# Kernel tuning notes

Hardware: AMD Instinct MI355X
Metric: run time of the kernel (lower is better)

Reference implementation:

```python
import jax, jax.numpy as jnp
import numpy as np

B, S, H, I, E = 2, 1024, 1024, 4096, 8

def setup_inputs() -> dict:
    key = jax.random.key(0)
    ks = jax.random.split(key, 8)
    s_h = 1.0 / np.sqrt(H)
    s_i = 1.0 / np.sqrt(I)
    return {
        "x": jax.random.normal(ks[0], (B, S, H), dtype=jnp.float32),
        "router_w": jax.random.uniform(ks[1], (H, E), jnp.float32, -s_h, s_h),
        "router_b": jax.random.uniform(ks[2], (E,), jnp.float32, -s_h, s_h),
        "w1": jax.random.uniform(ks[3], (E, H, I), jnp.float32, -s_h, s_h),
        "b1": jax.random.uniform(ks[4], (E, I), jnp.float32, -s_h, s_h),
        "w2": jax.random.uniform(ks[5], (E, I, H), jnp.float32, -s_i, s_i),
        "b2": jax.random.uniform(ks[6], (E, H), jnp.float32, -s_i, s_i),
        "game_emb": jax.random.normal(ks[7], (E, H), dtype=jnp.float32) * 0.02,
    }

def reference(x, router_w, router_b, w1, b1, w2, b2, game_emb):
    # Router: top-1 expert per token (softmax is monotone, argmax of logits)
    logits = jnp.einsum('bsh,he->bse', x, router_w) + router_b  # [B,S,E]
    expert_idx = jnp.argmax(logits, axis=-1)                    # [B,S] int
    out = jnp.zeros_like(x)
    n_experts = w1.shape[0]
    for e in range(n_experts):  # fixed small expert loop
        mask = (expert_idx == e)[..., None]                     # [B,S,1]
        sel = x + 0.1 * game_emb[e]                             # embedding add
        h = jax.nn.gelu(jnp.einsum('bsh,hi->bsi', sel, w1[e]) + b1[e], approximate=False)
        y = jnp.einsum('bsi,ih->bsh', h, w2[e]) + b2[e]
        out = jnp.where(mask, y, out)                           # scatter combine
    return out
```

## Files before the change

### kernel.cpp

```cpp
#include <hip/hip_runtime.h>
#include <hip/hip_bf16.h>
#include <math.h>

#define HDIM 1024
#define IDIM 4096
#define NE 8
#define NTOK 2048
#define PADROWS 256

typedef __attribute__((ext_vector_type(8))) short bf16x8;
typedef __attribute__((ext_vector_type(4))) float f32x4;

__device__ __forceinline__ unsigned int f2bf(float f) {
    unsigned int u = __float_as_uint(f);
    u = (u + 0x7FFFu + ((u >> 16) & 1u)) >> 16;
    return u;
}

__device__ __forceinline__ unsigned int pkbf2(float lo, float hi) {
    union { __hip_bfloat162 h; unsigned int u; } cv;
    cv.h = __float22bfloat162_rn(make_float2(lo, hi));
    return cv.u;
}

__device__ __forceinline__ float comp4(const float4& v, int c) {
    return c == 0 ? v.x : c == 1 ? v.y : c == 2 ? v.z : v.w;
}

__device__ __forceinline__ int swz8(int i) { return (i ^ (i >> 3)) & 7; }

__device__ __forceinline__ float gelu_erf(float v) {
    float x = v * 0.70710678118654752f;
    float ax = fabsf(x);
    float t = 1.0f / (1.0f + 0.3275911f * ax);
    float p = t * (0.254829592f + t * (-0.284496736f + t * (1.421413741f +
              t * (-1.453152027f + t * 1.061405429f))));
    float er = 1.0f - p * __expf(-x * x);
    er = copysignf(er, v);
    return 0.5f * v * (1.0f + er);
}

template<typename T, typename U>
__device__ __forceinline__ void gld16(const T* g, U* l) {
    __builtin_amdgcn_global_load_lds((const __attribute__((address_space(1))) void*)g,
                                     (__attribute__((address_space(3))) void*)l, 16, 0, 0);
}

__global__ __launch_bounds__(256) void router_k(const float* __restrict__ x,
                                                const float* __restrict__ rw,
                                                const float* __restrict__ rb,
                                                int* __restrict__ eidx,
                                                int* __restrict__ counts) {
    const int wave = threadIdx.x >> 6, lane = threadIdx.x & 63;
    const int t = blockIdx.x * 4 + wave;
    if (t >= NTOK) return;
    double acc[NE];
#pragma unroll
    for (int e = 0; e < NE; e++) acc[e] = 0.0;
    for (int h = lane; h < HDIM; h += 64) {
        double xv = (double)x[(size_t)t * HDIM + h];
        const float4* rwp = (const float4*)&rw[h * NE];
        float4 r0 = rwp[0], r1 = rwp[1];
        acc[0] += xv * (double)r0.x;  acc[1] += xv * (double)r0.y;
        acc[2] += xv * (double)r0.z;  acc[3] += xv * (double)r0.w;
        acc[4] += xv * (double)r1.x;  acc[5] += xv * (double)r1.y;
        acc[6] += xv * (double)r1.z;  acc[7] += xv * (double)r1.w;
    }
#pragma unroll
    for (int m = 32; m >= 1; m >>= 1) {
#pragma unroll
        for (int e = 0; e < NE; e++) acc[e] += __shfl_xor(acc[e], m);
    }
    if (lane == 0) {
        double best = acc[0] + (double)rb[0];
        int be = 0;
#pragma unroll
        for (int e = 1; e < NE; e++) {
            double v = acc[e] + (double)rb[e];
            if (v > best) { best = v; be = e; }
        }
        eidx[t] = be;
        atomicAdd(&counts[be], 1);
    }
}

__global__ void scan_k(const int* __restrict__ counts, int* __restrict__ offsets) {
    if (threadIdx.x == 0 && blockIdx.x == 0) {
        int s = 0;
        for (int e = 0; e < NE; e++) { offsets[e] = s; s += counts[e]; }
        offsets[NE] = s;
    }
}

__global__ __launch_bounds__(256) void gather_k(const float* __restrict__ x,
                                                const float* __restrict__ gemb,
                                                const int* __restrict__ eidx,
                                                const int* __restrict__ offsets,
                                                int* __restrict__ cursors,
                                                int* __restrict__ rowmap,
                                                unsigned short* __restrict__ Xg) {
    __shared__ int srow, se;
    const int t = blockIdx.x;
    if (threadIdx.x == 0) {
        int e = eidx[t];
        int pos = atomicAdd(&cursors[e], 1);
        int row = offsets[e] + pos;
        rowmap[row] = t;
        srow = row; se = e;
    }
    __syncthreads();
    const int row = srow, e = se;
    const int c = threadIdx.x * 4;
    float4 xv = *(const float4*)&x[(size_t)t * HDIM + c];
    float4 gv = *(const float4*)&gemb[(size_t)e * HDIM + c];
    ushort4 o;
    o.x = (unsigned short)f2bf(xv.x + 0.1f * gv.x);
    o.y = (unsigned short)f2bf(xv.y + 0.1f * gv.y);
    o.z = (unsigned short)f2bf(xv.z + 0.1f * gv.z);
    o.w = (unsigned short)f2bf(xv.w + 0.1f * gv.w);
    *(ushort4*)&Xg[(size_t)row * HDIM + c] = o;
}

template<int EPI>
__global__ __launch_bounds__(1024, 4) void moe_gemm_k(
        const unsigned short* __restrict__ A, int lda, int Kfull, int ksplit,
        const float* __restrict__ Bw, int ldbN,
        const float* __restrict__ bias,
        const int* __restrict__ offsets, const int* __restrict__ rowmap,
        unsigned short* __restrict__ Hout, float* __restrict__ Yout,
        float* __restrict__ P, size_t pstride, int ncb, int nsp) {
    __shared__ __align__(16) unsigned short At[2][256 * 64];
    __shared__ __align__(16) unsigned short Bt[128 * 64];

    const int bid = blockIdx.x;
    const int e = bid & 7;
    int loc = bid >> 3;
    const int cblk = loc % ncb;  loc /= ncb;
    const int split = loc % nsp;
    const int yblk = loc / nsp;

    const int rend = offsets[e + 1];
    const int r0 = offsets[e] + yblk * 256;
    if (r0 >= rend) return;
    const int c0 = cblk * 128;
    const int kbeg = split * ksplit;
    const int nt = ksplit / 64;
    const float* Be = Bw + (size_t)e * Kfull * ldbN;

    const int tid = threadIdx.x;
    const int wave = tid >> 6, lane = tid & 63;
    const int wr = (wave >> 2) * 64;
    const int wc = (wave & 3) * 32;
    const int l15 = lane & 15, l4 = lane >> 4;

    const int cg = tid & 31, kid = tid >> 5;
    const int bcol = cg * 4;
    const int boct = kid >> 2;
    const int brow = (kid * 2) & 7;
    const float* bsrc = Be + (size_t)(kid * 2) * ldbN + c0 + bcol;
    int bwo[4];
#pragma unroll
    for (int i = 0; i < 4; ++i) {
        int col = bcol + i;
        bwo[i] = col * 64 + (boct ^ swz8(col)) * 8 + brow;
    }

    const unsigned short* adsrc[2];
    int adoff[2];
#pragma unroll
    for (int p = 0; p < 2; ++p) {
        int gidx = p * 1024 + tid;
        int row = gidx >> 3, ps = gidx & 7;
        adsrc[p] = A + (size_t)(r0 + row) * lda + (ps ^ swz8(row)) * 8;
        adoff[p] = gidx * 8;
    }

    float4 fv[2];
    auto loadB = [&](int kabs) {
#pragma unroll
        for (int j = 0; j < 2; ++j)
            fv[j] = *(const float4*)&bsrc[(size_t)(kabs + j) * ldbN];
    };
    auto dmaA = [&](int kabs, int buf) {
#pragma unroll
        for (int p = 0; p < 2; ++p)
            gld16(adsrc[p] + kabs, &At[buf][adoff[p]]);
    };

    f32x4 acc[4][2];
#pragma unroll
    for (int m = 0; m < 4; ++m)
#pragma unroll
        for (int n = 0; n < 2; ++n) acc[m][n] = (f32x4){0.f, 0.f, 0.f, 0.f};

    loadB(kbeg);
    dmaA(kbeg, 0);
    for (int t = 0; t < nt; ++t) {
        const int cur = t & 1;
#pragma unroll
        for (int i = 0; i < 4; ++i)
            *(unsigned int*)&Bt[bwo[i]] = pkbf2(comp4(fv[0], i), comp4(fv[1], i));
        if (t + 1 < nt) {
            loadB(kbeg + (t + 1) * 64);
            dmaA(kbeg + (t + 1) * 64, cur ^ 1);
            asm volatile("s_waitcnt vmcnt(4) lgkmcnt(0)" ::: "memory");
        } else {
            asm volatile("s_waitcnt vmcnt(0) lgkmcnt(0)" ::: "memory");
        }
        __builtin_amdgcn_s_barrier();
        __builtin_amdgcn_sched_barrier(0);
#pragma unroll
        for (int kh = 0; kh < 2; ++kh) {
            const int kb = kh * 4 + l4;
            bf16x8 af[4], bfr[2];
#pragma unroll
            for (int m = 0; m < 4; ++m) {
                int row = wr + m * 16 + l15;
                af[m] = *(const bf16x8*)&At[cur][row * 64 + (kb ^ swz8(row)) * 8];
            }
#pragma unroll
            for (int n = 0; n < 2; ++n) {
                int col = wc + n * 16 + l15;
                bfr[n] = *(const bf16x8*)&Bt[col * 64 + (kb ^ swz8(col)) * 8];
            }
#pragma unroll
            for (int m = 0; m < 4; ++m)
#pragma unroll
                for (int n = 0; n < 2; ++n)
                    acc[m][n] = __builtin_amdgcn_mfma_f32_16x16x32_bf16(af[m], bfr[n], acc[m][n], 0, 0, 0);
        }
        __builtin_amdgcn_sched_barrier(0);
        __builtin_amdgcn_s_barrier();
        __builtin_amdgcn_sched_barrier(0);
    }

#pragma unroll
    for (int m = 0; m < 4; ++m) {
#pragma unroll
        for (int r = 0; r < 4; ++r) {
            const int row = r0 + wr + m * 16 + l4 * 4 + r;
            if (row < rend) {
                if constexpr (EPI == 0) {
#pragma unroll
                    for (int n = 0; n < 2; ++n) {
                        int col = c0 + wc + n * 16 + l15;
                        float v = acc[m][n][r] + bias[(size_t)e * ldbN + col];
                        Hout[(size_t)row * IDIM + col] = (unsigned short)f2bf(gelu_erf(v));
                    }
                } else if (split == 0) {
                    const int tt = rowmap[row];
#pragma unroll
                    for (int n = 0; n < 2; ++n) {
                        int col = c0 + wc + n * 16 + l15;
                        Yout[(size_t)tt * HDIM + col] = acc[m][n][r] + bias[(size_t)e * ldbN + col];
                    }
                } else {
                    float* Ps = P + (size_t)(split - 1) * pstride;
#pragma unroll
                    for (int n = 0; n < 2; ++n) {
                        int col = c0 + wc + n * 16 + l15;
                        Ps[(size_t)row * HDIM + col] = acc[m][n][r];
                    }
                }
            }
        }
    }
}

__global__ __launch_bounds__(256) void reduce_k(const float* __restrict__ P,
                                                size_t pstride, int nparts,
                                                const int* __restrict__ rowmap,
                                                float* __restrict__ out) {
    const int row = blockIdx.x;
    const int t = rowmap[row];
    const int c = threadIdx.x * 4;
    f32x4 s = *(const f32x4*)&out[(size_t)t * HDIM + c];
    for (int p = 0; p < nparts; ++p)
        s += *(const f32x4*)&P[(size_t)p * pstride + (size_t)row * HDIM + c];
    *(f32x4*)&out[(size_t)t * HDIM + c] = s;
}

extern "C" void kernel_launch(void* const* d_in, const int* in_sizes, int n_in,
                              void* d_out, int out_size, void* d_ws, size_t ws_size,
                              hipStream_t stream) {
    const float* x    = (const float*)d_in[0];
    const float* rw   = (const float*)d_in[1];
    const float* rb   = (const float*)d_in[2];
    const float* w1   = (const float*)d_in[3];
    const float* b1   = (const float*)d_in[4];
    const float* w2   = (const float*)d_in[5];
    const float* b2   = (const float*)d_in[6];
    const float* gemb = (const float*)d_in[7];
    float* out = (float*)d_out;

    char* ws = (char*)d_ws;
    int* meta    = (int*)ws;
    int* counts  = meta;
    int* cursors = meta + 8;
    int* offsets = meta + 16;
    int* eidx    = meta + 32;
    int* rowmap  = meta + 32 + NTOK;
    size_t off = 32768;
    unsigned short* Xg = (unsigned short*)(ws + off);
    off += (size_t)(NTOK + PADROWS) * HDIM * 2;
    unsigned short* Hbuf = (unsigned short*)(ws + off);
    off += (size_t)(NTOK + PADROWS) * IDIM * 2;
    float* P = (float*)(ws + off);
    const size_t pstride = (size_t)NTOK * HDIM;
    int nsplit = 1;
    if (ws_size >= off + 3 * pstride * 4) nsplit = 4;
    else if (ws_size >= off + 1 * pstride * 4) nsplit = 2;

    hipMemsetAsync(counts, 0, 16 * sizeof(int), stream);
    router_k<<<NTOK / 4, 256, 0, stream>>>(x, rw, rb, eidx, counts);
    scan_k<<<1, 64, 0, stream>>>(counts, offsets);
    gather_k<<<NTOK, 256, 0, stream>>>(x, gemb, eidx, offsets, cursors, rowmap, Xg);
    moe_gemm_k<0><<<512, 1024, 0, stream>>>(
        Xg, HDIM, HDIM, HDIM, w1, IDIM, b1, offsets, rowmap,
        Hbuf, nullptr, nullptr, 0, 32, 1);
    moe_gemm_k<1><<<8 * 8 * nsplit * 2, 1024, 0, stream>>>(
        Hbuf, IDIM, IDIM, IDIM / nsplit, w2, HDIM, b2, offsets, rowmap,
        nullptr, out, P, pstride, 8, nsplit);
    if (nsplit > 1)
        reduce_k<<<NTOK, 256, 0, stream>>>(P, pstride, nsplit - 1, rowmap, out);
}
```

Before: 209.1 us.

## Load A fragments directly from global and double-buffer converted B tile in LDS

The A operand no longer goes through LDS via global_load_lds DMA; each wave now reads its bf16 A fragments straight from global memory into registers for the MFMA. The B (fp32 weight) tile is now double-buffered in LDS with a two-stage register prefetch, leaving one barrier per k-step instead of two. The aim is to cut LDS traffic and synchronisation, at the cost of uncoalesced, unhidden global latency on the A loads, which are repeated by the four waves that share the same rows.

```diff
diff --git a/kernel.cpp b/kernel.cpp
--- a/kernel.cpp
+++ b/kernel.cpp
@@ -23,9 +23,7 @@
     return cv.u;
 }
 
-__device__ __forceinline__ float comp4(const float4& v, int c) {
-    return c == 0 ? v.x : c == 1 ? v.y : c == 2 ? v.z : v.w;
-}
+__device__ __forceinline__ float comp2(const float2& v, int i) { return i ? v.y : v.x; }
 
 __device__ __forceinline__ int swz8(int i) { return (i ^ (i >> 3)) & 7; }
 
@@ -38,12 +36,6 @@
     float er = 1.0f - p * __expf(-x * x);
     er = copysignf(er, v);
     return 0.5f * v * (1.0f + er);
-}
-
-template<typename T, typename U>
-__device__ __forceinline__ void gld16(const T* g, U* l) {
-    __builtin_amdgcn_global_load_lds((const __attribute__((address_space(1))) void*)g,
-                                     (__attribute__((address_space(3))) void*)l, 16, 0, 0);
 }
 
 __global__ __launch_bounds__(256) void router_k(const float* __restrict__ x,
@@ -129,8 +121,7 @@
         const int* __restrict__ offsets, const int* __restrict__ rowmap,
         unsigned short* __restrict__ Hout, float* __restrict__ Yout,
         float* __restrict__ P, size_t pstride, int ncb, int nsp) {
-    __shared__ __align__(16) unsigned short At[2][256 * 64];
-    __shared__ __align__(16) unsigned short Bt[128 * 64];
+    __shared__ __align__(16) unsigned short Bt[2][128 * 64];
 
     const int bid = blockIdx.x;
     const int e = bid & 7;
@@ -153,38 +144,34 @@
     const int wc = (wave & 3) * 32;
     const int l15 = lane & 15, l4 = lane >> 4;
 
-    const int cg = tid & 31, kid = tid >> 5;
-    const int bcol = cg * 4;
-    const int boct = kid >> 2;
-    const int brow = (kid * 2) & 7;
-    const float* bsrc = Be + (size_t)(kid * 2) * ldbN + c0 + bcol;
-    int bwo[4];
-#pragma unroll
-    for (int i = 0; i < 4; ++i) {
-        int col = bcol + i;
-        bwo[i] = col * 64 + (boct ^ swz8(col)) * 8 + brow;
-    }
-
-    const unsigned short* adsrc[2];
-    int adoff[2];
-#pragma unroll
-    for (int p = 0; p < 2; ++p) {
-        int gidx = p * 1024 + tid;
-        int row = gidx >> 3, ps = gidx & 7;
-        adsrc[p] = A + (size_t)(r0 + row) * lda + (ps ^ swz8(row)) * 8;
-        adoff[p] = gidx * 8;
-    }
-
-    float4 fv[2];
-    auto loadB = [&](int kabs) {
-#pragma unroll
-        for (int j = 0; j < 2; ++j)
-            fv[j] = *(const float4*)&bsrc[(size_t)(kabs + j) * ldbN];
+    const int oct = wave >> 1, sub = wave & 1;
+    const float* bsrc = Be + (size_t)(kbeg + wave * 4) * ldbN + c0 + lane * 2;
+    int bwo[2];
+#pragma unroll
+    for (int i = 0; i < 2; ++i) {
+        int col = lane * 2 + i;
+        bwo[i] = col * 64 + ((oct ^ swz8(col)) << 3) + sub * 4;
+    }
+
+    const unsigned short* arow[4];
+#pragma unroll
+    for (int m = 0; m < 4; ++m)
+        arow[m] = A + (size_t)(r0 + wr + m * 16 + l15) * lda + kbeg;
+
+    float2 fv[4];
+    auto loadB = [&](int koff) {
+#pragma unroll
+        for (int j = 0; j < 4; ++j)
+            fv[j] = *(const float2*)&bsrc[(size_t)(koff + j) * ldbN];
     };
-    auto dmaA = [&](int kabs, int buf) {
-#pragma unroll
-        for (int p = 0; p < 2; ++p)
-            gld16(adsrc[p] + kabs, &At[buf][adoff[p]]);
+    auto writeB = [&](int buf) {
+#pragma unroll
+        for (int i = 0; i < 2; ++i) {
+            uint2 w;
+            w.x = pkbf2(comp2(fv[0], i), comp2(fv[1], i));
+            w.y = pkbf2(comp2(fv[2], i), comp2(fv[3], i));
+            *(uint2*)&Bt[buf][bwo[i]] = w;
+        }
     };
 
     f32x4 acc[4][2];
@@ -193,35 +180,26 @@
 #pragma unroll
         for (int n = 0; n < 2; ++n) acc[m][n] = (f32x4){0.f, 0.f, 0.f, 0.f};
 
-    loadB(kbeg);
-    dmaA(kbeg, 0);
+    loadB(0);
+    writeB(0);
+    if (nt > 1) loadB(64);
+    asm volatile("s_waitcnt lgkmcnt(0)" ::: "memory");
+    __builtin_amdgcn_s_barrier();
+    __builtin_amdgcn_sched_barrier(0);
+
     for (int t = 0; t < nt; ++t) {
         const int cur = t & 1;
-#pragma unroll
-        for (int i = 0; i < 4; ++i)
-            *(unsigned int*)&Bt[bwo[i]] = pkbf2(comp4(fv[0], i), comp4(fv[1], i));
-        if (t + 1 < nt) {
-            loadB(kbeg + (t + 1) * 64);
-            dmaA(kbeg + (t + 1) * 64, cur ^ 1);
-            asm volatile("s_waitcnt vmcnt(4) lgkmcnt(0)" ::: "memory");
-        } else {
-            asm volatile("s_waitcnt vmcnt(0) lgkmcnt(0)" ::: "memory");
-        }
-        __builtin_amdgcn_s_barrier();
-        __builtin_amdgcn_sched_barrier(0);
 #pragma unroll
         for (int kh = 0; kh < 2; ++kh) {
             const int kb = kh * 4 + l4;
             bf16x8 af[4], bfr[2];
 #pragma unroll
-            for (int m = 0; m < 4; ++m) {
-                int row = wr + m * 16 + l15;
-                af[m] = *(const bf16x8*)&At[cur][row * 64 + (kb ^ swz8(row)) * 8];
-            }
+            for (int m = 0; m < 4; ++m)
+                af[m] = *(const bf16x8*)&arow[m][t * 64 + kb * 8];
 #pragma unroll
             for (int n = 0; n < 2; ++n) {
                 int col = wc + n * 16 + l15;
-                bfr[n] = *(const bf16x8*)&Bt[col * 64 + (kb ^ swz8(col)) * 8];
+                bfr[n] = *(const bf16x8*)&Bt[cur][col * 64 + ((kb ^ swz8(col)) << 3)];
             }
 #pragma unroll
             for (int m = 0; m < 4; ++m)
@@ -229,9 +207,13 @@
                 for (int n = 0; n < 2; ++n)
                     acc[m][n] = __builtin_amdgcn_mfma_f32_16x16x32_bf16(af[m], bfr[n], acc[m][n], 0, 0, 0);
         }
-        __builtin_amdgcn_sched_barrier(0);
-        __builtin_amdgcn_s_barrier();
-        __builtin_amdgcn_sched_barrier(0);
+        if (t + 1 < nt) {
+            writeB(cur ^ 1);
+            if (t + 2 < nt) loadB((t + 2) * 64);
+            asm volatile("s_waitcnt lgkmcnt(0)" ::: "memory");
+            __builtin_amdgcn_s_barrier();
+            __builtin_amdgcn_sched_barrier(0);
+        }
     }
 
 #pragma unroll
```

New measurement: 363.6 us. +73.9%, slower.
